# Kernel optimization log

Hardware: AMD Instinct MI355X
Metric: run time of the kernel (lower is better)

## Reference

```python
import jax, jax.numpy as jnp
import numpy as np


def silu(x):
    return x * jax.nn.sigmoid(x)


def setup_inputs() -> dict:
    key = jax.random.key(0)
    ks = jax.random.split(key, 12)
    B, S, Dm = 2, 2048, 768
    I, N, R, K = 1536, 16, 48, 4
    s = 0.02
    return {
        "input_states": jax.random.normal(ks[0], (B, S, Dm), jnp.float32),
        "in_proj_w": jax.random.normal(ks[1], (2 * I, Dm), jnp.float32) * s,
        "conv_w": jax.random.normal(ks[2], (I, 1, K), jnp.float32) * s,
        "conv_b": jax.random.normal(ks[3], (I,), jnp.float32) * s,
        "x_proj_w": jax.random.normal(ks[4], (R + 2 * N, I), jnp.float32) * s,
        "dt_proj_w": jax.random.normal(ks[5], (I, R), jnp.float32) * s,
        "dt_proj_b": jax.random.normal(ks[6], (I,), jnp.float32) * s,
        "A_log": jax.random.normal(ks[7], (I, N), jnp.float32) * 0.5,
        "D": jax.random.normal(ks[8], (I,), jnp.float32) * s,
        "out_proj_w": jax.random.normal(ks[9], (Dm, I), jnp.float32) * s,
        "alpha": jax.random.uniform(ks[10], (I,), jnp.float32),
        "feature_gating": jax.random.uniform(ks[11], (I,), jnp.float32),
    }


def reference(input_states, in_proj_w, conv_w, conv_b, x_proj_w,
              dt_proj_w, dt_proj_b, A_log, D, out_proj_w,
              alpha, feature_gating):
    Bsz, S, _ = input_states.shape
    I, N = A_log.shape
    R = dt_proj_w.shape[1]
    K = conv_w.shape[-1]

    # in_proj (no bias), chunk into hidden / gate, each [B, I, S]
    proj = jnp.einsum('bsd,ed->bse', input_states, in_proj_w)  # [B, S, 2I]
    hidden, gate = jnp.split(proj.transpose(0, 2, 1), 2, axis=1)

    # causal depthwise conv1d + SiLU
    h = jax.lax.conv_general_dilated(
        hidden, conv_w, window_strides=(1,), padding=[(K - 1, 0)],
        dimension_numbers=('NCH', 'OIH', 'NCH'), feature_group_count=I)
    h = silu(h + conv_b[None, :, None])  # [B, I, S]

    # x_proj -> time_step, B, C
    ssm_p = jnp.einsum('bis,ei->bse', h, x_proj_w)  # [B, S, R+2N]
    ts, Bm, Cm = jnp.split(ssm_p, [R, R + N], axis=-1)

    dt = jax.nn.softplus(jnp.einsum('bsr,ir->bsi', ts, dt_proj_w) + dt_proj_b)
    dt = dt.transpose(0, 2, 1)                       # [B, I, S]
    dt = dt.at[:, :, -1].multiply(alpha[None, :])    # alpha scales last step

    A = -jnp.exp(A_log.astype(jnp.float32))          # [I, N]
    dA = jnp.exp(A[None, :, None, :] * dt[:, :, :, None])       # [B, I, S, N]
    dBu = dt[:, :, :, None] * Bm[:, None, :, :] * h[:, :, :, None]  # [B, I, S, N]

    def step(state, xs):
        dA_t, dBu_t, C_t = xs
        state = dA_t * state + dBu_t                 # [B, I, N]
        y = jnp.einsum('bin,bn->bi', state, C_t)
        return state, y

    init = jnp.zeros((Bsz, I, N), input_states.dtype)
    _, ys = jax.lax.scan(
        step, init,
        (dA.transpose(2, 0, 1, 3), dBu.transpose(2, 0, 1, 3), Cm.transpose(1, 0, 2)))
    y = ys.transpose(1, 2, 0)                        # [B, I, S]

    y = (y + h * D[None, :, None]) * silu(gate)
    y = y.at[:, :, -1].multiply(feature_gating[None, :])
    return jnp.einsum('bis,di->bsd', y, out_proj_w)  # [B, S, Dm]
```

## Files before the change

kernel.cpp:

```cpp
#include <hip/hip_runtime.h>
#include <math.h>


static constexpr int S_LEN  = 2048;
static constexpr int DMODEL = 768;
static constexpr int ICH    = 1536;
static constexpr int NST    = 16;
static constexpr int MROWS  = 4096;
static constexpr int NCH    = 64;
static constexpr int CHS    = 32;
static constexpr int CSTR   = 2 * ICH * NST;

typedef _Float16 f16;
typedef f16 f16x8 __attribute__((ext_vector_type(8)));
typedef f16 f16x4 __attribute__((ext_vector_type(4)));
typedef f16 f16x2 __attribute__((ext_vector_type(2)));
typedef float f32x4 __attribute__((ext_vector_type(4)));

#if __has_builtin(__builtin_amdgcn_exp2f)
#define EXP2F(x) __builtin_amdgcn_exp2f(x)
#else
#define EXP2F(x) exp2f(x)
#endif

typedef __attribute__((address_space(3))) void lds_void;
typedef const __attribute__((address_space(1))) void glb_void;

__device__ __forceinline__ void glds16(f16* l, const f16* g) {
    __builtin_amdgcn_global_load_lds((glb_void*)g, (lds_void*)l, 16, 0, 0);
}

__device__ __forceinline__ float silu_f(float x) {
    return x / (1.0f + __expf(-x));
}

__global__ __launch_bounds__(256) void cvt2(
    const float* __restrict__ s0, f16* __restrict__ d0, int n0,
    const float* __restrict__ s1, f16* __restrict__ d1)
{
    int i = (blockIdx.x * 256 + threadIdx.x) * 4;
    const float* s; f16* d;
    if (i < n0)            { s = s0 + i;        d = d0 + i; }
    else                   { s = s1 + (i - n0); d = d1 + (i - n0); }
    float4 v = *(const float4*)s;
    f16x4 o = { (f16)v.x, (f16)v.y, (f16)v.z, (f16)v.w };
    *(f16x4*)d = o;
}

__global__ __launch_bounds__(256) void k1m(
    const f16* __restrict__ Xh,
    const f16* __restrict__ Wh,
    f16* __restrict__ hidden,
    f16* __restrict__ sgate)
{
    __shared__ __align__(16) f16 As[2][128 * 32];
    __shared__ __align__(16) f16 Bs[2][128 * 32];
    const int tid = threadIdx.x;
    const int lane = tid & 63, wave = tid >> 6;
    const int quad = lane >> 4, l16 = lane & 15;
    const int wm = wave & 1, wn = wave >> 1;
    const int m0 = blockIdx.x * 128, n0 = blockIdx.y * 128;
    const int l_row = lane >> 2, l_c8 = (lane & 3) * 8;

    const f16* Ag = Xh + (size_t)(m0 + wave * 16 + l_row) * 768 + l_c8;
    const f16* Bg = Wh + (size_t)(n0 + wave * 16 + l_row) * 768 + l_c8;
    const int sLo = (wave * 16) * 32, sHi = (64 + wave * 16) * 32;

#define K1_STAGE(buf, kk)                                        \
    do {                                                         \
        glds16(&As[buf][sLo], Ag + (kk));                        \
        glds16(&As[buf][sHi], Ag + (size_t)64 * 768 + (kk));     \
        glds16(&Bs[buf][sLo], Bg + (kk));                        \
        glds16(&Bs[buf][sHi], Bg + (size_t)64 * 768 + (kk));     \
    } while (0)

#define K1_COMPUTE(buf)                                                        \
    do {                                                                       \
        f16x8 af[4], bf[4];                                                    \
        _Pragma("unroll")                                                      \
        for (int mi = 0; mi < 4; ++mi)                                         \
            af[mi] = *(const f16x8*)&As[buf][(wm * 64 + mi * 16 + l16) * 32 + quad * 8]; \
        _Pragma("unroll")                                                      \
        for (int ni = 0; ni < 4; ++ni)                                         \
            bf[ni] = *(const f16x8*)&Bs[buf][(wn * 64 + ni * 16 + l16) * 32 + quad * 8]; \
        _Pragma("unroll")                                                      \
        for (int mi = 0; mi < 4; ++mi)                                         \
            _Pragma("unroll")                                                  \
            for (int ni = 0; ni < 4; ++ni)                                     \
                acc[mi][ni] = __builtin_amdgcn_mfma_f32_16x16x32_f16(          \
                    af[mi], bf[ni], acc[mi][ni], 0, 0, 0);                     \
    } while (0)

    K1_STAGE(0, 0);
    __syncthreads();

    f32x4 acc[4][4] = {};
    for (int k0 = 0; k0 < 768; k0 += 64) {
        K1_STAGE(1, k0 + 32);
        K1_COMPUTE(0);
        __syncthreads();
        if (k0 + 64 < 768) K1_STAGE(0, k0 + 64);
        K1_COMPUTE(1);
        __syncthreads();
    }
#undef K1_STAGE
#undef K1_COMPUTE

    const bool isGate = (n0 >= ICH);
    f16* outp = isGate ? sgate : hidden;
    const int e0 = (isGate ? (n0 - ICH) : n0) + wn * 64 + l16;
    #pragma unroll
    for (int mi = 0; mi < 4; ++mi) {
        #pragma unroll
        for (int ni = 0; ni < 4; ++ni) {
            #pragma unroll
            for (int r = 0; r < 4; ++r) {
                int m = m0 + wm * 64 + mi * 16 + quad * 4 + r;
                int e = e0 + ni * 16;
                float v = acc[mi][ni][r];
                if (isGate) v = silu_f(v);
                outp[(size_t)m * ICH + e] = (f16)v;
            }
        }
    }
}

__global__ __launch_bounds__(256) void k3m(
    const f16* __restrict__ hidden,
    const float* __restrict__ conv_w,
    const float* __restrict__ conv_b,
    const float* __restrict__ xw,
    f16* __restrict__ h,
    float* __restrict__ ssmp)
{
    __shared__ __align__(16) f16 Ah[128 * 32];
    __shared__ __align__(16) f16 Bh[80 * 32];
    __shared__ float4 cwv[96];
    __shared__ float  cbv[96];
    const int tid = threadIdx.x;
    const int lane = tid & 63, wave = tid >> 6;
    const int quad = lane >> 4, l16 = lane & 15;
    const int m0 = blockIdx.x * 128;
    const int kbeg = blockIdx.y * 96;

    if (tid < 96) {
        cwv[tid] = *(const float4*)(conv_w + (size_t)(kbeg + tid) * 4);
        cbv[tid] = conv_b[kbeg + tid];
    }

    f32x4 acc[2][5] = {};
    for (int k0 = kbeg; k0 < kbeg + 96; k0 += 32) {
        __syncthreads();
        #pragma unroll
        for (int it = 0; it < 2; ++it) {
            int slot = tid + it * 256;
            int r_ = slot >> 2, c_ = (slot & 3) * 8;
            int gm = m0 + r_, c = k0 + c_;
            int s = gm & (S_LEN - 1);
            const f16* bp = hidden + (size_t)gm * ICH + c;
            f16x8 x0 = *(const f16x8*)bp;
            f16x8 x1 = *(const f16x8*)(bp - (s >= 1 ? ICH : 0));
            f16x8 x2 = *(const f16x8*)(bp - (s >= 2 ? 2 * ICH : 0));
            f16x8 x3 = *(const f16x8*)(bp - (s >= 3 ? 3 * ICH : 0));
            f16x8 o;
            #pragma unroll
            for (int j = 0; j < 8; ++j) {
                int ci = (k0 - kbeg) + c_ + j;
                float4 w = cwv[ci];
                float v1 = (s >= 1) ? (float)x1[j] : 0.f;
                float v2 = (s >= 2) ? (float)x2[j] : 0.f;
                float v3 = (s >= 3) ? (float)x3[j] : 0.f;
                float r = cbv[ci] + w.x * v3 + w.y * v2 + w.z * v1 + w.w * (float)x0[j];
                o[j] = (f16)silu_f(r);
            }
            *(f16x8*)&Ah[r_ * 32 + c_] = o;
            *(f16x8*)(h + (size_t)gm * ICH + c) = o;
        }
        {
            int c4 = (tid & 7) * 4;
            for (int r = tid >> 3; r < 80; r += 32) {
                float4 v = *(const float4*)(xw + (size_t)r * ICH + k0 + c4);
                f16x4 o = { (f16)v.x, (f16)v.y, (f16)v.z, (f16)v.w };
                *(f16x4*)&Bh[r * 32 + c4] = o;
            }
        }
        __syncthreads();
        f16x8 af[2], bf[5];
        #pragma unroll
        for (int mi = 0; mi < 2; ++mi)
            af[mi] = *(const f16x8*)&Ah[(wave * 32 + mi * 16 + l16) * 32 + quad * 8];
        #pragma unroll
        for (int j = 0; j < 5; ++j)
            bf[j] = *(const f16x8*)&Bh[(j * 16 + l16) * 32 + quad * 8];
        #pragma unroll
        for (int mi = 0; mi < 2; ++mi)
            #pragma unroll
            for (int j = 0; j < 5; ++j)
                acc[mi][j] = __builtin_amdgcn_mfma_f32_16x16x32_f16(
                    af[mi], bf[j], acc[mi][j], 0, 0, 0);
    }
    #pragma unroll
    for (int mi = 0; mi < 2; ++mi) {
        #pragma unroll
        for (int j = 0; j < 5; ++j) {
            #pragma unroll
            for (int r = 0; r < 4; ++r) {
                int m = m0 + wave * 32 + mi * 16 + quad * 4 + r;
                atomicAdd(ssmp + (size_t)m * 80 + j * 16 + l16, acc[mi][j][r]);
            }
        }
    }
}

__global__ __launch_bounds__(256) void k4m(
    const float* __restrict__ ssmp,
    const float* __restrict__ dtw,
    const float* __restrict__ dtb,
    const float* __restrict__ alpha,
    f16* __restrict__ dt)
{
    __shared__ __align__(16) f16 As[128 * 72];
    __shared__ __align__(16) f16 Bs[128 * 72];
    const int tid = threadIdx.x;
    const int lane = tid & 63, wave = tid >> 6;
    const int quad = lane >> 4, l16 = lane & 15;
    const int wm = wave & 1, wn = wave >> 1;
    const int m0 = blockIdx.x * 128, n0 = blockIdx.y * 128;
    const int srow = tid >> 1;
    const int shalf = tid & 1;

    {
        const float* sa = ssmp + (size_t)(m0 + srow) * 80 + shalf * 24;
        const float* sb = dtw + (size_t)(n0 + srow) * 48 + shalf * 24;
        f16* da = &As[srow * 72 + shalf * 24];
        f16* db = &Bs[srow * 72 + shalf * 24];
        #pragma unroll
        for (int j = 0; j < 6; ++j) {
            float4 va = *(const float4*)(sa + 4 * j);
            float4 vb = *(const float4*)(sb + 4 * j);
            f16x4 oa = { (f16)va.x, (f16)va.y, (f16)va.z, (f16)va.w };
            f16x4 ob = { (f16)vb.x, (f16)vb.y, (f16)vb.z, (f16)vb.w };
            *(f16x4*)(da + 4 * j) = oa;
            *(f16x4*)(db + 4 * j) = ob;
        }
        if (shalf) {
            f16x8 z = {};
            *(f16x8*)&As[srow * 72 + 48] = z;
            *(f16x8*)&As[srow * 72 + 56] = z;
            *(f16x8*)&Bs[srow * 72 + 48] = z;
            *(f16x8*)&Bs[srow * 72 + 56] = z;
        }
    }
    __syncthreads();

    f32x4 acc[4][4] = {};
    #pragma unroll
    for (int ks = 0; ks < 2; ++ks) {
        f16x8 af[4], bf[4];
        #pragma unroll
        for (int mi = 0; mi < 4; ++mi)
            af[mi] = *(const f16x8*)&As[(wm * 64 + mi * 16 + l16) * 72 + ks * 32 + quad * 8];
        #pragma unroll
        for (int ni = 0; ni < 4; ++ni)
            bf[ni] = *(const f16x8*)&Bs[(wn * 64 + ni * 16 + l16) * 72 + ks * 32 + quad * 8];
        #pragma unroll
        for (int mi = 0; mi < 4; ++mi)
            #pragma unroll
            for (int ni = 0; ni < 4; ++ni)
                acc[mi][ni] = __builtin_amdgcn_mfma_f32_16x16x32_f16(
                    af[mi], bf[ni], acc[mi][ni], 0, 0, 0);
    }

    #pragma unroll
    for (int ni = 0; ni < 4; ++ni) {
        int e = n0 + wn * 64 + ni * 16 + l16;
        float bias = dtb[e];
        float al = alpha[e];
        #pragma unroll
        for (int mi = 0; mi < 4; ++mi) {
            #pragma unroll
            for (int r = 0; r < 4; ++r) {
                int m = m0 + wm * 64 + mi * 16 + quad * 4 + r;
                float x = acc[mi][ni][r] + bias;
                float sp = (x > 20.0f) ? x : __logf(1.0f + __expf(x));
                if ((m & (S_LEN - 1)) == S_LEN - 1) sp *= al;
                dt[(size_t)m * ICH + e] = (f16)sp;
            }
        }
    }
}

__global__ __launch_bounds__(256) void k5a_chunk(
    const f16* __restrict__ dt,
    const f16* __restrict__ h,
    const float* __restrict__ ssmp,
    const float* __restrict__ A_log,
    float* __restrict__ PArr,
    float* __restrict__ SfArr)
{
    __shared__ float dts[CHS * 64];
    __shared__ float hs[CHS * 64];
    __shared__ float Bc[CHS][16];
    const int tid = threadIdx.x;
    const int n4 = tid & 3;
    const int il = tid >> 2;
    const int i0 = blockIdx.x * 64;
    const int i = i0 + il;
    const int c = blockIdx.y;
    const int b = blockIdx.z;
    const int s0 = c * CHS;
    const size_t row0 = (size_t)(b * S_LEN + s0) * ICH + i0;

    {
        int r = tid >> 3, c8 = (tid & 7) * 8;
        size_t g_off = row0 + (size_t)r * ICH + c8;
        f16x8 dv = *(const f16x8*)(dt + g_off);
        f16x8 hv = *(const f16x8*)(h + g_off);
        #pragma unroll
        for (int j = 0; j < 8; ++j) {
            dts[r * 64 + c8 + j] = (float)dv[j];
            hs[r * 64 + c8 + j]  = (float)hv[j];
        }
    }
    if (tid < CHS * 4) {
        int t = tid >> 2, q = tid & 3;
        *(float4*)&Bc[t][q * 4] =
            *(const float4*)(ssmp + (size_t)(b * S_LEN + s0 + t) * 80 + 48 + q * 4);
    }

    const float L2E = 1.44269504088896f;
    float4 alv = *(const float4*)(A_log + i * NST + n4 * 4);
    float A[4] = { -__expf(alv.x) * L2E, -__expf(alv.y) * L2E,
                   -__expf(alv.z) * L2E, -__expf(alv.w) * L2E };
    float st[4] = {};
    float cdt = 0.f;
    __syncthreads();
    #pragma unroll 4
    for (int t = 0; t < CHS; ++t) {
        float dtv = dts[t * 64 + il];
        float hv  = hs[t * 64 + il];
        float4 Bv = *(const float4*)&Bc[t][n4 * 4];
        cdt += dtv;
        float x = dtv * hv;
        #pragma unroll
        for (int j = 0; j < 4; ++j) {
            float dA = EXP2F(A[j] * dtv);
            st[j] = fmaf(dA, st[j], x * (&Bv.x)[j]);
        }
    }
    size_t base = (size_t)c * CSTR + (size_t)(b * ICH + i) * NST + n4 * 4;
    float4 Pv = { EXP2F(A[0] * cdt), EXP2F(A[1] * cdt),
                  EXP2F(A[2] * cdt), EXP2F(A[3] * cdt) };
    float4 Sv = { st[0], st[1], st[2], st[3] };
    *(float4*)(PArr + base)  = Pv;
    *(float4*)(SfArr + base) = Sv;
}

__global__ __launch_bounds__(256) void k5b_carry(
    const float* PArr,
    const float* __restrict__ SfArr,
    float* CIn)
{
    int idx = blockIdx.x * 256 + threadIdx.x;
    float p[NCH], s[NCH];
    #pragma unroll
    for (int c = 0; c < NCH; ++c) {
        size_t a = (size_t)c * CSTR + idx;
        p[c] = PArr[a];
        s[c] = SfArr[a];
    }
    float carry = 0.f;
    #pragma unroll
    for (int c = 0; c < NCH; ++c) {
        CIn[(size_t)c * CSTR + idx] = carry;
        carry = fmaf(p[c], carry, s[c]);
    }
}

__global__ __launch_bounds__(256) void k5c_emit(
    const f16* __restrict__ dt,
    const f16* __restrict__ h,
    const f16* __restrict__ sgate,
    const float* __restrict__ ssmp,
    const float* __restrict__ A_log,
    const float* __restrict__ Dp,
    const float* __restrict__ fg,
    const float* __restrict__ CIn,
    f16* __restrict__ yh)
{
    __shared__ float dts[CHS * 64];
    __shared__ float hs[CHS * 64];
    __shared__ float gs[CHS * 64];
    __shared__ float BC[CHS][32];
    const int tid = threadIdx.x;
    const int n4 = tid & 3;
    const int il = tid >> 2;
    const int i0 = blockIdx.x * 64;
    const int i = i0 + il;
    const int c = blockIdx.y;
    const int b = blockIdx.z;
    const int s0 = c * CHS;
    const size_t row0 = (size_t)(b * S_LEN + s0) * ICH + i0;

    {
        int r = tid >> 3, c8 = (tid & 7) * 8;
        size_t g_off = row0 + (size_t)r * ICH + c8;
        f16x8 dv = *(const f16x8*)(dt + g_off);
        f16x8 hv = *(const f16x8*)(h + g_off);
        f16x8 gv = *(const f16x8*)(sgate + g_off);
        #pragma unroll
        for (int j = 0; j < 8; ++j) {
            dts[r * 64 + c8 + j] = (float)dv[j];
            hs[r * 64 + c8 + j]  = (float)hv[j];
            gs[r * 64 + c8 + j]  = (float)gv[j];
        }
    }
    {
        int t = tid >> 3, q = tid & 7;
        *(float4*)&BC[t][q * 4] =
            *(const float4*)(ssmp + (size_t)(b * S_LEN + s0 + t) * 80 + 48 + q * 4);
    }

    const float L2E = 1.44269504088896f;
    float4 alv = *(const float4*)(A_log + i * NST + n4 * 4);
    float A[4] = { -__expf(alv.x) * L2E, -__expf(alv.y) * L2E,
                   -__expf(alv.z) * L2E, -__expf(alv.w) * L2E };
    const float Dv = Dp[i];
    const float fgv = fg[i];
    float4 civ = *(const float4*)(CIn + (size_t)c * CSTR + (size_t)(b * ICH + i) * NST + n4 * 4);
    float st[4] = { civ.x, civ.y, civ.z, civ.w };
    f16* yout = yh + row0 + il;
    const bool last_chunk = (c == NCH - 1);
    __syncthreads();
    #pragma unroll 4
    for (int t = 0; t < CHS; ++t) {
        float dtv = dts[t * 64 + il];
        float hv  = hs[t * 64 + il];
        float4 Bv = *(const float4*)&BC[t][n4 * 4];
        float4 Cv = *(const float4*)&BC[t][16 + n4 * 4];
        float x = dtv * hv;
        float yp = 0.f;
        #pragma unroll
        for (int j = 0; j < 4; ++j) {
            float dA = EXP2F(A[j] * dtv);
            st[j] = fmaf(dA, st[j], x * (&Bv.x)[j]);
            yp = fmaf(st[j], (&Cv.x)[j], yp);
        }
        yp += __shfl_xor(yp, 1, 4);
        yp += __shfl_xor(yp, 2, 4);
        if (n4 == 0) {
            float yv = fmaf(hv, Dv, yp) * gs[t * 64 + il];
            if (last_chunk && t == CHS - 1) yv *= fgv;
            yout[(size_t)t * ICH] = (f16)yv;
        }
    }
}

__global__ __launch_bounds__(256) void k6m(
    const f16* __restrict__ Yh,
    const float* __restrict__ OWf,
    float* __restrict__ out)
{
    __shared__ __align__(16) f16 As[2][64 * 32];
    __shared__ __align__(16) f16 Bs[2][64 * 32];
    const int tid = threadIdx.x;
    const int lane = tid & 63, wave = tid >> 6;
    const int quad = lane >> 4, l16 = lane & 15;
    const int wm = wave & 1, wn = wave >> 1;
    const int m0 = blockIdx.x * 64, n0 = blockIdx.y * 64;
    const int l_row = lane >> 2, l_c8 = (lane & 3) * 8;

    const f16* Ag = Yh + (size_t)(m0 + wave * 16 + l_row) * ICH + l_c8;
    const int aOff = (wave * 16) * 32;
    const int brow = tid >> 2, bc8 = (tid & 3) * 8;
    const float* Bgf = OWf + (size_t)(n0 + brow) * ICH + bc8;
    float4 vb0, vb1;

#define K6_STAGEA(buf, kk) glds16(&As[buf][aOff], Ag + (kk))

#define K6_LOADB(kk)                                             \
    do {                                                         \
        vb0 = *(const float4*)(Bgf + (kk));                      \
        vb1 = *(const float4*)(Bgf + (kk) + 4);                  \
    } while (0)

#define K6_WRITEB(buf)                                                         \
    do {                                                                       \
        f16x8 o = { (f16)vb0.x, (f16)vb0.y, (f16)vb0.z, (f16)vb0.w,            \
                    (f16)vb1.x, (f16)vb1.y, (f16)vb1.z, (f16)vb1.w };          \
        *(f16x8*)&Bs[buf][brow * 32 + bc8] = o;                                \
    } while (0)

#define K6_COMPUTE(buf)                                                        \
    do {                                                                       \
        f16x8 af[2], bf[2];                                                    \
        _Pragma("unroll")                                                      \
        for (int mi = 0; mi < 2; ++mi)                                         \
            af[mi] = *(const f16x8*)&As[buf][(wm * 32 + mi * 16 + l16) * 32 + quad * 8]; \
        _Pragma("unroll")                                                      \
        for (int ni = 0; ni < 2; ++ni)                                         \
            bf[ni] = *(const f16x8*)&Bs[buf][(wn * 32 + ni * 16 + l16) * 32 + quad * 8]; \
        _Pragma("unroll")                                                      \
        for (int mi = 0; mi < 2; ++mi)                                         \
            _Pragma("unroll")                                                  \
            for (int ni = 0; ni < 2; ++ni)                                     \
                acc[mi][ni] = __builtin_amdgcn_mfma_f32_16x16x32_f16(          \
                    af[mi], bf[ni], acc[mi][ni], 0, 0, 0);                     \
    } while (0)

    K6_STAGEA(0, 0);
    K6_LOADB(0);
    K6_WRITEB(0);
    __syncthreads();

    f32x4 acc[2][2] = {};
    for (int k0 = 0; k0 < ICH; k0 += 64) {
        K6_STAGEA(1, k0 + 32);
        K6_LOADB(k0 + 32);
        K6_COMPUTE(0);
        K6_WRITEB(1);
        __syncthreads();
        if (k0 + 64 < ICH) {
            K6_STAGEA(0, k0 + 64);
            K6_LOADB(k0 + 64);
        }
        K6_COMPUTE(1);
        if (k0 + 64 < ICH) K6_WRITEB(0);
        __syncthreads();
    }
#undef K6_STAGEA
#undef K6_LOADB
#undef K6_WRITEB
#undef K6_COMPUTE

    #pragma unroll
    for (int mi = 0; mi < 2; ++mi) {
        #pragma unroll
        for (int ni = 0; ni < 2; ++ni) {
            #pragma unroll
            for (int r = 0; r < 4; ++r) {
                int m = m0 + wm * 32 + mi * 16 + quad * 4 + r;
                int d = n0 + wn * 32 + ni * 16 + l16;
                out[(size_t)m * DMODEL + d] = acc[mi][ni][r];
            }
        }
    }
}

extern "C" void kernel_launch(void* const* d_in, const int* in_sizes, int n_in,
                              void* d_out, int out_size, void* d_ws, size_t ws_size,
                              hipStream_t stream) {
    const float* X     = (const float*)d_in[0];
    const float* W1    = (const float*)d_in[1];
    const float* CW    = (const float*)d_in[2];
    const float* CB    = (const float*)d_in[3];
    const float* XW    = (const float*)d_in[4];
    const float* DTW   = (const float*)d_in[5];
    const float* DTB   = (const float*)d_in[6];
    const float* ALOG  = (const float*)d_in[7];
    const float* DD    = (const float*)d_in[8];
    const float* OW    = (const float*)d_in[9];
    const float* ALPHA = (const float*)d_in[10];
    const float* FG    = (const float*)d_in[11];
    float* out = (float*)d_out;

    const size_t NBI = (size_t)MROWS * ICH;
    f16* hidden_h = (f16*)d_ws;
    f16* sgate_h  = hidden_h + NBI;
    f16* h_h      = sgate_h + NBI;
    f16* dt_h     = h_h + NBI;
    float* ssmp   = (float*)(dt_h + NBI);
    f16* Xh       = (f16*)(ssmp + (size_t)MROWS * 80);
    f16* W1h      = Xh + (size_t)MROWS * DMODEL;
    float* SfA    = (float*)(W1h + (size_t)2 * ICH * DMODEL);
    float* PArr = (float*)hidden_h;
    float* CIn  = PArr;
    f16* yh     = (f16*)SfA;

    const int nX = MROWS * DMODEL, nW1 = 2 * ICH * DMODEL;
    hipMemsetAsync(ssmp, 0, (size_t)MROWS * 80 * sizeof(float), stream);
    cvt2<<<dim3((nX + nW1) / 1024), 256, 0, stream>>>(X, Xh, nX, W1, W1h);
    k1m<<<dim3(32, 24), 256, 0, stream>>>(Xh, W1h, hidden_h, sgate_h);
    k3m<<<dim3(32, 16), 256, 0, stream>>>(hidden_h, CW, CB, XW, h_h, ssmp);
    k4m<<<dim3(32, 12), 256, 0, stream>>>(ssmp, DTW, DTB, ALPHA, dt_h);
    k5a_chunk<<<dim3(24, NCH, 2), 256, 0, stream>>>(dt_h, h_h, ssmp, ALOG, PArr, SfA);
    k5b_carry<<<dim3(192), 256, 0, stream>>>(PArr, SfA, CIn);
    k5c_emit<<<dim3(24, NCH, 2), 256, 0, stream>>>(dt_h, h_h, sgate_h, ssmp, ALOG, DD, FG, CIn, yh);
    k6m<<<dim3(64, 12), 256, 0, stream>>>(yh, OW, out);
}
```

Before: 242.9 us.

## Fold chunk carry scan into emit kernel and merge memset into prep

Removes the separate carry-propagation kernel. Each emit block now recomputes its incoming state by serially scanning the per-chunk decay and final-state arrays of all earlier chunks. The zeroing of the ssm projection buffer moves from a memset into the conversion kernel, saving launches. The cost is redundant work: later chunks read up to 63 prior chunk records each, which adds global traffic and latency to the emit kernel.

Measured after the change: 253.2 us. +4.3%, slower.

```diff
diff --git a/kernel.cpp b/kernel.cpp
--- a/kernel.cpp
+++ b/kernel.cpp
@@ -34,17 +34,26 @@
     return x / (1.0f + __expf(-x));
 }
 
-__global__ __launch_bounds__(256) void cvt2(
+__global__ __launch_bounds__(256) void prep(
     const float* __restrict__ s0, f16* __restrict__ d0, int n0,
-    const float* __restrict__ s1, f16* __restrict__ d1)
+    const float* __restrict__ s1, f16* __restrict__ d1, int n1,
+    float* __restrict__ z)
 {
     int i = (blockIdx.x * 256 + threadIdx.x) * 4;
-    const float* s; f16* d;
-    if (i < n0)            { s = s0 + i;        d = d0 + i; }
-    else                   { s = s1 + (i - n0); d = d1 + (i - n0); }
-    float4 v = *(const float4*)s;
-    f16x4 o = { (f16)v.x, (f16)v.y, (f16)v.z, (f16)v.w };
-    *(f16x4*)d = o;
+    if (i < n0) {
+        float4 v = *(const float4*)(s0 + i);
+        f16x4 o = { (f16)v.x, (f16)v.y, (f16)v.z, (f16)v.w };
+        *(f16x4*)(d0 + i) = o;
+    } else if (i < n0 + n1) {
+        int j = i - n0;
+        float4 v = *(const float4*)(s1 + j);
+        f16x4 o = { (f16)v.x, (f16)v.y, (f16)v.z, (f16)v.w };
+        *(f16x4*)(d1 + j) = o;
+    } else {
+        int j = i - n0 - n1;
+        float4 zv = {};
+        *(float4*)(z + j) = zv;
+    }
 }
 
 __global__ __launch_bounds__(256) void k1m(
@@ -356,27 +365,6 @@
     *(float4*)(SfArr + base) = Sv;
 }
 
-__global__ __launch_bounds__(256) void k5b_carry(
-    const float* PArr,
-    const float* __restrict__ SfArr,
-    float* CIn)
-{
-    int idx = blockIdx.x * 256 + threadIdx.x;
-    float p[NCH], s[NCH];
-    #pragma unroll
-    for (int c = 0; c < NCH; ++c) {
-        size_t a = (size_t)c * CSTR + idx;
-        p[c] = PArr[a];
-        s[c] = SfArr[a];
-    }
-    float carry = 0.f;
-    #pragma unroll
-    for (int c = 0; c < NCH; ++c) {
-        CIn[(size_t)c * CSTR + idx] = carry;
-        carry = fmaf(p[c], carry, s[c]);
-    }
-}
-
 __global__ __launch_bounds__(256) void k5c_emit(
     const f16* __restrict__ dt,
     const f16* __restrict__ h,
@@ -385,7 +373,8 @@
     const float* __restrict__ A_log,
     const float* __restrict__ Dp,
     const float* __restrict__ fg,
-    const float* __restrict__ CIn,
+    const float* __restrict__ PArr,
+    const float* __restrict__ SfArr,
     f16* __restrict__ yh)
 {
     __shared__ float dts[CHS * 64];
@@ -427,8 +416,21 @@
                    -__expf(alv.z) * L2E, -__expf(alv.w) * L2E };
     const float Dv = Dp[i];
     const float fgv = fg[i];
-    float4 civ = *(const float4*)(CIn + (size_t)c * CSTR + (size_t)(b * ICH + i) * NST + n4 * 4);
-    float st[4] = { civ.x, civ.y, civ.z, civ.w };
+
+    float st[4] = {};
+    {
+        const size_t sbase = (size_t)(b * ICH + i) * NST + n4 * 4;
+        for (int cc = 0; cc < c; ++cc) {
+            size_t a = (size_t)cc * CSTR + sbase;
+            float4 p = *(const float4*)(PArr + a);
+            float4 s = *(const float4*)(SfArr + a);
+            st[0] = fmaf(p.x, st[0], s.x);
+            st[1] = fmaf(p.y, st[1], s.y);
+            st[2] = fmaf(p.z, st[2], s.z);
+            st[3] = fmaf(p.w, st[3], s.w);
+        }
+    }
+
     f16* yout = yh + row0 + il;
     const bool last_chunk = (c == NCH - 1);
     __syncthreads();
@@ -574,17 +576,16 @@
     f16* W1h      = Xh + (size_t)MROWS * DMODEL;
     float* SfA    = (float*)(W1h + (size_t)2 * ICH * DMODEL);
     float* PArr = (float*)hidden_h;
-    float* CIn  = PArr;
-    f16* yh     = (f16*)SfA;
-
-    const int nX = MROWS * DMODEL, nW1 = 2 * ICH * DMODEL;
-    hipMemsetAsync(ssmp, 0, (size_t)MROWS * 80 * sizeof(float), stream);
-    cvt2<<<dim3((nX + nW1) / 1024), 256, 0, stream>>>(X, Xh, nX, W1, W1h);
+    f16* yh     = Xh;
+
+    const int nX = MROWS * DMODEL;
+    const int nW1 = 2 * ICH * DMODEL;
+    const int nS = MROWS * 80;
+    prep<<<dim3((nX + nW1 + nS) / 1024), 256, 0, stream>>>(X, Xh, nX, W1, W1h, nW1, ssmp);
     k1m<<<dim3(32, 24), 256, 0, stream>>>(Xh, W1h, hidden_h, sgate_h);
     k3m<<<dim3(32, 16), 256, 0, stream>>>(hidden_h, CW, CB, XW, h_h, ssmp);
     k4m<<<dim3(32, 12), 256, 0, stream>>>(ssmp, DTW, DTB, ALPHA, dt_h);
     k5a_chunk<<<dim3(24, NCH, 2), 256, 0, stream>>>(dt_h, h_h, ssmp, ALOG, PArr, SfA);
-    k5b_carry<<<dim3(192), 256, 0, stream>>>(PArr, SfA, CIn);
-    k5c_emit<<<dim3(24, NCH, 2), 256, 0, stream>>>(dt_h, h_h, sgate_h, ssmp, ALOG, DD, FG, CIn, yh);
+    k5c_emit<<<dim3(24, NCH, 2), 256, 0, stream>>>(dt_h, h_h, sgate_h, ssmp, ALOG, DD, FG, PArr, SfA, yh);
     k6m<<<dim3(64, 12), 256, 0, stream>>>(yh, OW, out);
 }
```
